# Optimization experiments

Measured on AMD Instinct MI355X. Metric: run time of the kernel, lower is better.

## Reference

```python
import jax, jax.numpy as jnp
import numpy as np

N = 50000          # nodes
E = 800000         # edges (before self-loops)
DIN = 1024         # input_dim_mel
HID = 128          # hidden_dim
HEADS = 2
NC = 4             # num_classes
NEG_SLOPE = 0.2    # PyG GATConv default


def setup_inputs() -> dict:
    key = jax.random.key(0)
    ks = jax.random.split(key, 12)
    s = 0.05
    return {
        "x": jax.random.normal(ks[0], (N, DIN), dtype=jnp.float32),
        "edge_index": jax.random.randint(ks[1], (2, E), 0, N, dtype=jnp.int64),
        # linear_pre (stored as [in, out])
        "W_pre": jax.random.normal(ks[2], (DIN, HID), dtype=jnp.float32) * s,
        "b_pre": jnp.zeros((HID,), dtype=jnp.float32),
        # gat1: GATConv(HID, HID, heads=2, concat=True)
        "W1": jax.random.normal(ks[3], (HID, HEADS * HID), dtype=jnp.float32) * s,
        "a_src1": jax.random.normal(ks[4], (HEADS, HID), dtype=jnp.float32) * s,
        "a_dst1": jax.random.normal(ks[5], (HEADS, HID), dtype=jnp.float32) * s,
        "b1": jnp.zeros((HEADS * HID,), dtype=jnp.float32),
        # gat2: GATConv(HID*HEADS, NC, heads=1, concat=True)
        "W2": jax.random.normal(ks[6], (HEADS * HID, NC), dtype=jnp.float32) * s,
        "a_src2": jax.random.normal(ks[7], (1, NC), dtype=jnp.float32) * s,
        "a_dst2": jax.random.normal(ks[8], (1, NC), dtype=jnp.float32) * s,
        "b2": jnp.zeros((NC,), dtype=jnp.float32),
    }


def _gat_conv(x, W, a_src, a_dst, bias, src, dst, heads, out_ch):
    """PyG GATConv (concat=True, self-loops already appended to src/dst)."""
    n = x.shape[0]
    h = (x @ W).reshape(n, heads, out_ch)            # [N,H,C]
    alpha_src = (h * a_src).sum(-1)                  # [N,H]
    alpha_dst = (h * a_dst).sum(-1)                  # [N,H]
    e = alpha_src[src] + alpha_dst[dst]              # [E,H] edge scores
    e = jax.nn.leaky_relu(e, NEG_SLOPE)
    # segment softmax over incoming edges of each dst node
    m = jax.ops.segment_max(e, dst, num_segments=n)  # [N,H]
    e = jnp.exp(e - m[dst])
    s = jax.ops.segment_sum(e, dst, num_segments=n)  # [N,H]
    alpha = e / (s[dst] + 1e-16)                     # [E,H]
    # gather src messages, weight by attention, scatter-add to dst
    out = jax.ops.segment_sum(h[src] * alpha[:, :, None], dst, num_segments=n)
    return out.reshape(n, heads * out_ch) + bias


def reference(x, edge_index, W_pre, b_pre, W1, a_src1, a_dst1, b1,
              W2, a_src2, a_dst2, b2):
    n = x.shape[0]
    # add self-loops (PyG GATConv default)
    loops = jnp.arange(n, dtype=edge_index.dtype)
    src = jnp.concatenate([edge_index[0], loops])
    dst = jnp.concatenate([edge_index[1], loops])

    h = jax.nn.relu(x @ W_pre + b_pre)                               # [N,HID]
    h = jax.nn.elu(_gat_conv(h, W1, a_src1, a_dst1, b1, src, dst, HEADS, HID))
    out = _gat_conv(h, W2, a_src2, a_dst2, b2, src, dst, 1, NC)      # [N,NC]
    return out
```

## Files before the change

kernel.cpp:

```cpp
#include <hip/hip_runtime.h>
#include <hip/hip_bf16.h>

#define NEG_SLOPE 0.2f

typedef _Float16 f16x8 __attribute__((ext_vector_type(8)));
typedef _Float16 f16x4 __attribute__((ext_vector_type(4)));
typedef float f32x4 __attribute__((ext_vector_type(4)));
typedef unsigned short ushort_t;

#define AS_GLOBAL(p) ((const __attribute__((address_space(1))) void*)(p))
#define AS_SHARED(p) ((__attribute__((address_space(3))) void*)(p))

__device__ inline f16x4 cvt4(float4 v) {
    f16x4 r;
    r[0] = (_Float16)v.x; r[1] = (_Float16)v.y;
    r[2] = (_Float16)v.z; r[3] = (_Float16)v.w;
    return r;
}

__global__ __launch_bounds__(256) void kl1(const int* __restrict__ edst, int E,
                                           int* __restrict__ counts,
                                           const float* __restrict__ Wpre,
                                           const float* __restrict__ W1,
                                           ushort_t* __restrict__ PreF,
                                           ushort_t* __restrict__ W1h, int HB) {
    int b = blockIdx.x, t = threadIdx.x;
    if (b < HB) {
        int i = b * 256 + t;
        if (i < E) atomicAdd(&counts[edst[i]], 1);
    } else {
        int i = (b - HB) * 256 + t;
        if (i < 1024 * 128) {
            int k = i >> 7, n = i & 127;
            int d = ((k >> 3) * 128 + n) * 8 + (k & 7);
            PreF[d] = __builtin_bit_cast(ushort_t, (_Float16)Wpre[i]);
        } else if (i < 1024 * 128 + 128 * 256) {
            int j2 = i - 1024 * 128;
            int k = j2 >> 8, n = j2 & 255;
            int d = ((k >> 3) * 256 + n) * 8 + (k & 7);
            W1h[d] = __builtin_bit_cast(ushort_t, (_Float16)W1[j2]);
        }
    }
}

__global__ __launch_bounds__(256) void kl2(const float* __restrict__ A,
                                           const ushort_t* __restrict__ Bf,
                                           const float* __restrict__ bias,
                                           ushort_t* __restrict__ C, int M,
                                           const int* __restrict__ counts,
                                           int* __restrict__ row_ptr,
                                           int* __restrict__ cursor) {
    __shared__ __align__(16) ushort_t Bs[8192];
    __shared__ __align__(16) ushort_t As[2048];
    __shared__ int wsum2[4];
    int t = threadIdx.x;

    if (blockIdx.x == 0) {
        int CH = (M + 255) >> 8;
        int lo = t * CH, hi = min(lo + CH, M);
        int s = 0;
        for (int i = lo; i < hi; ++i) s += counts[i] + 1;
        int lane = t & 63, wid = t >> 6;
        int x = s;
        #pragma unroll
        for (int off = 1; off < 64; off <<= 1) {
            int y = __shfl_up(x, off, 64);
            if (lane >= off) x += y;
        }
        if (lane == 63) wsum2[wid] = x;
        __syncthreads();
        int wof = 0;
        #pragma unroll
        for (int w = 0; w < 3; ++w) if (wid > w) wof += wsum2[w];
        int run = wof + x - s;
        for (int i = lo; i < hi; ++i) {
            row_ptr[i] = run;
            cursor[i] = run;
            run += counts[i] + 1;
        }
        if (lo < M && hi == M) row_ptr[M] = run;
        return;
    }

    int wid = t >> 6, lane = t & 63, q = lane >> 4, l15 = lane & 15;
    int wr = wid & 1, wc = wid >> 1;
    int m0 = (blockIdx.x - 1) * 32;

    int ar = t >> 3, ac = t & 7;
    int srow = m0 + ar;
    if (srow >= M) srow = M - 1;
    const float* sA = A + (size_t)srow * 1024;
    int sw = ar & 7;
    int wadr0 = ar * 64 + (((ac >> 1)) ^ sw) * 8 + (ac & 1) * 4;
    int wadr1 = ar * 64 + ((4 + (ac >> 1)) ^ sw) * 8 + (ac & 1) * 4;

    float4 av[2][2];
    av[0][0] = *(const float4*)(sA + ac * 4);
    av[0][1] = *(const float4*)(sA + 32 + ac * 4);

    f32x4 acc[4];
    #pragma unroll
    for (int c = 0; c < 4; ++c) acc[c] = (f32x4){0.f, 0.f, 0.f, 0.f};

    int arow_rd = (wr * 16 + l15) * 64;
    int asw = l15 & 7;

    #pragma unroll 2
    for (int kt = 0; kt < 16; ++kt) {
        int cur = kt & 1, nxt = cur ^ 1;
        __syncthreads();
        {
            const ushort_t* sF = Bf + kt * 8192;
            #pragma unroll
            for (int i = 0; i < 4; ++i) {
                int ge = (i * 256 + t) * 8;
                int le = (i * 256 + (t & 0xC0)) * 8;
                __builtin_amdgcn_global_load_lds(AS_GLOBAL(sF + ge), AS_SHARED(Bs + le), 16, 0, 0);
            }
        }
        if (kt < 15) {
            const float* a2 = sA + (kt + 1) * 64;
            av[nxt][0] = *(const float4*)(a2 + ac * 4);
            av[nxt][1] = *(const float4*)(a2 + 32 + ac * 4);
        }
        *(f16x4*)(As + wadr0) = cvt4(av[cur][0]);
        *(f16x4*)(As + wadr1) = cvt4(av[cur][1]);
        __syncthreads();
        #pragma unroll
        for (int ks = 0; ks < 2; ++ks) {
            int kc = ks * 4 + q;
            f16x8 af = *(const f16x8*)(As + arow_rd + ((kc ^ asw) * 8));
            #pragma unroll
            for (int c = 0; c < 4; ++c) {
                f16x8 b = *(const f16x8*)(Bs + (kc * 128 + wc * 64 + c * 16 + l15) * 8);
                acc[c] = __builtin_amdgcn_mfma_f32_16x16x32_f16(af, b, acc[c], 0, 0, 0);
            }
        }
    }
    #pragma unroll
    for (int c = 0; c < 4; ++c) {
        int n = wc * 64 + c * 16 + l15;
        float bv = bias[n];
        #pragma unroll
        for (int r = 0; r < 4; ++r) {
            int mm = m0 + wr * 16 + q * 4 + r;
            if (mm < M)
                C[(size_t)mm * 128 + n] =
                    __builtin_bit_cast(ushort_t, (_Float16)fmaxf(acc[c][r] + bv, 0.f));
        }
    }
}

__global__ __launch_bounds__(256) void kl3(const int* __restrict__ esrc,
                                           const int* __restrict__ edst, int E, int n,
                                           int* __restrict__ cursor,
                                           int* __restrict__ edge_src, int FB,
                                           const ushort_t* __restrict__ Ah,
                                           const ushort_t* __restrict__ W1h,
                                           const float* __restrict__ a_src,
                                           const float* __restrict__ a_dst,
                                           ushort_t* __restrict__ C,
                                           float* __restrict__ as1,
                                           float* __restrict__ ad1, int M) {
    __shared__ __align__(16) ushort_t Bs[16384];
    int t = threadIdx.x;
    int b = blockIdx.x;
    if (b < FB) {
        int i = b * 256 + t;
        if (i < E) {
            int p = atomicAdd(&cursor[edst[i]], 1);
            edge_src[p] = esrc[i];
        } else if (i < E + n) {
            int v = i - E;
            int p = atomicAdd(&cursor[v], 1);
            edge_src[p] = v;
        }
        return;
    }
    int u = b - FB;
    int g = u & 1;
    int mblk = u >> 1;
    int wid = t >> 6, lane = t & 63;
    int q = lane >> 4, l15 = lane & 15;
    int m0 = mblk * 64 + wid * 16;
    int m = m0 + l15;
    const ushort_t* arow = Ah + (size_t)(m < M ? m : 0) * 128;

    {
        #pragma unroll
        for (int i = 0; i < 8; ++i) {
            int j = i * 4 + wid;
            int kc = j >> 1, hk = j & 1;
            int ge = ((kc * 256) + g * 128 + hk * 64 + lane) * 8;
            int le = j * 512;
            __builtin_amdgcn_global_load_lds(AS_GLOBAL(W1h + ge), AS_SHARED(Bs + le), 16, 0, 0);
        }
    }
    f16x8 af[4];
    #pragma unroll
    for (int ks = 0; ks < 4; ++ks)
        af[ks] = *(const f16x8*)(arow + ks * 32 + q * 8);
    __syncthreads();

    f32x4 acc[8];
    #pragma unroll
    for (int c = 0; c < 8; ++c) acc[c] = (f32x4){0.f, 0.f, 0.f, 0.f};

    #pragma unroll
    for (int ks = 0; ks < 4; ++ks) {
        int kc = ks * 4 + q;
        #pragma unroll
        for (int c = 0; c < 8; ++c) {
            f16x8 bfr = *(const f16x8*)(Bs + (kc * 128 + c * 16 + l15) * 8);
            acc[c] = __builtin_amdgcn_mfma_f32_16x16x32_f16(af[ks], bfr, acc[c], 0, 0, 0);
        }
    }
    #pragma unroll
    for (int c = 0; c < 8; ++c) {
        int nn = g * 128 + c * 16 + l15;
        #pragma unroll
        for (int r = 0; r < 4; ++r) {
            int mm = m0 + q * 4 + r;
            if (mm < M)
                C[(size_t)mm * 256 + nn] = __builtin_bit_cast(ushort_t, (_Float16)acc[c][r]);
        }
    }
    float asv[4] = {0.f, 0.f, 0.f, 0.f};
    float adv[4] = {0.f, 0.f, 0.f, 0.f};
    #pragma unroll
    for (int c = 0; c < 8; ++c) {
        float sa = a_src[g * 128 + c * 16 + l15];
        float da = a_dst[g * 128 + c * 16 + l15];
        #pragma unroll
        for (int r = 0; r < 4; ++r) {
            asv[r] += acc[c][r] * sa;
            adv[r] += acc[c][r] * da;
        }
    }
    #pragma unroll
    for (int off = 1; off <= 8; off <<= 1) {
        #pragma unroll
        for (int r = 0; r < 4; ++r) {
            asv[r] += __shfl_xor(asv[r], off, 64);
            adv[r] += __shfl_xor(adv[r], off, 64);
        }
    }
    if (l15 == 0) {
        #pragma unroll
        for (int r = 0; r < 4; ++r) {
            int node = m0 + q * 4 + r;
            if (node < M) {
                as1[node * 2 + g] = asv[r];
                ad1[node * 2 + g] = adv[r];
            }
        }
    }
}

__global__ __launch_bounds__(256) void kagg1(const ushort_t* __restrict__ h1h,
                                             const float* __restrict__ as1,
                                             const float* __restrict__ ad1,
                                             const float* __restrict__ b1,
                                             const float* __restrict__ W2,
                                             const float* __restrict__ a_src2,
                                             const float* __restrict__ a_dst2,
                                             const int* __restrict__ row_ptr,
                                             const int* __restrict__ edge_src,
                                             float* __restrict__ h2,
                                             float* __restrict__ as2,
                                             float* __restrict__ ad2, int n) {
    int wid = threadIdx.x >> 6, lane = threadIdx.x & 63;
    int node = blockIdx.x * 4 + wid;
    if (node >= n) return;
    int beg = row_ptr[node], end = row_ptr[node + 1];
    int h = lane >> 5;
    float adv0 = ad1[node * 2];
    float adv1 = ad1[node * 2 + 1];
    float acc0 = 0.f, acc1 = 0.f, acc2 = 0.f, acc3 = 0.f, ssum = 0.f;
    for (int base = beg; base < end; base += 32) {
        int cnt = min(32, end - base);
        float wv_mine = 0.f;
        int s_mine = 0;
        {
            int i = lane >> 1, hh = lane & 1;
            if (i < cnt) {
                s_mine = edge_src[base + i];
                float e = as1[s_mine * 2 + hh] + (hh ? adv1 : adv0);
                e = (e > 0.f) ? e : NEG_SLOPE * e;
                wv_mine = __expf(e);
            }
        }
        #pragma unroll 4
        for (int i2 = 0; i2 < cnt; ++i2) {
            int s = __shfl(s_mine, i2 * 2, 64);
            float wv = __shfl(wv_mine, i2 * 2 + h, 64);
            uint2 p = *(const uint2*)(h1h + (size_t)s * 256 + lane * 4);
            acc0 += wv * (float)__builtin_bit_cast(_Float16, (ushort_t)(p.x & 0xffffu));
            acc1 += wv * (float)__builtin_bit_cast(_Float16, (ushort_t)(p.x >> 16));
            acc2 += wv * (float)__builtin_bit_cast(_Float16, (ushort_t)(p.y & 0xffffu));
            acc3 += wv * (float)__builtin_bit_cast(_Float16, (ushort_t)(p.y >> 16));
            ssum += wv;
        }
    }
    float inv = 1.f / (ssum + 1e-16f);
    float o0 = acc0 * inv + b1[lane * 4 + 0];
    float o1 = acc1 * inv + b1[lane * 4 + 1];
    float o2 = acc2 * inv + b1[lane * 4 + 2];
    float o3 = acc3 * inv + b1[lane * 4 + 3];
    o0 = (o0 > 0.f) ? o0 : (__expf(o0) - 1.f);
    o1 = (o1 > 0.f) ? o1 : (__expf(o1) - 1.f);
    o2 = (o2 > 0.f) ? o2 : (__expf(o2) - 1.f);
    o3 = (o3 > 0.f) ? o3 : (__expf(o3) - 1.f);
    float4 w0 = *(const float4*)(W2 + (lane * 4 + 0) * 4);
    float4 w1 = *(const float4*)(W2 + (lane * 4 + 1) * 4);
    float4 w2 = *(const float4*)(W2 + (lane * 4 + 2) * 4);
    float4 w3 = *(const float4*)(W2 + (lane * 4 + 3) * 4);
    float p0 = o0 * w0.x + o1 * w1.x + o2 * w2.x + o3 * w3.x;
    float p1 = o0 * w0.y + o1 * w1.y + o2 * w2.y + o3 * w3.y;
    float p2 = o0 * w0.z + o1 * w1.z + o2 * w2.z + o3 * w3.z;
    float p3 = o0 * w0.w + o1 * w1.w + o2 * w2.w + o3 * w3.w;
    #pragma unroll
    for (int off = 1; off < 64; off <<= 1) {
        p0 += __shfl_xor(p0, off, 64);
        p1 += __shfl_xor(p1, off, 64);
        p2 += __shfl_xor(p2, off, 64);
        p3 += __shfl_xor(p3, off, 64);
    }
    if (lane == 0) {
        h2[node * 4 + 0] = p0;
        h2[node * 4 + 1] = p1;
        h2[node * 4 + 2] = p2;
        h2[node * 4 + 3] = p3;
        as2[node] = p0 * a_src2[0] + p1 * a_src2[1] + p2 * a_src2[2] + p3 * a_src2[3];
        ad2[node] = p0 * a_dst2[0] + p1 * a_dst2[1] + p2 * a_dst2[2] + p3 * a_dst2[3];
    }
}

__global__ __launch_bounds__(256) void kagg2(const float* __restrict__ h2,
                                             const float* __restrict__ as2,
                                             const float* __restrict__ ad2,
                                             const float* __restrict__ b2,
                                             const int* __restrict__ row_ptr,
                                             const int* __restrict__ edge_src,
                                             float* __restrict__ out, int n) {
    int wid = threadIdx.x >> 6, lane = threadIdx.x & 63;
    int node = blockIdx.x * 4 + wid;
    if (node >= n) return;
    int beg = row_ptr[node], end = row_ptr[node + 1];
    int j = lane & 3, ig = lane >> 2;
    float adv = ad2[node];
    float acc = 0.f, ssum = 0.f;
    for (int p = beg + ig; p < end; p += 16) {
        int s = edge_src[p];
        float e = as2[s] + adv;
        e = (e > 0.f) ? e : NEG_SLOPE * e;
        float wv = __expf(e);
        acc += wv * h2[s * 4 + j];
        ssum += wv;
    }
    #pragma unroll
    for (int off = 32; off >= 4; off >>= 1) {
        acc += __shfl_down(acc, off);
        ssum += __shfl_down(ssum, off);
    }
    if (lane < 4) out[node * 4 + j] = acc / (ssum + 1e-16f) + b2[j];
}

extern "C" void kernel_launch(void* const* d_in, const int* in_sizes, int n_in,
                              void* d_out, int out_size, void* d_ws, size_t ws_size,
                              hipStream_t stream) {
    const float* x      = (const float*)d_in[0];
    const int*   ei     = (const int*)d_in[1];
    const float* W_pre  = (const float*)d_in[2];
    const float* b_pre  = (const float*)d_in[3];
    const float* W1     = (const float*)d_in[4];
    const float* a_src1 = (const float*)d_in[5];
    const float* a_dst1 = (const float*)d_in[6];
    const float* b1     = (const float*)d_in[7];
    const float* W2     = (const float*)d_in[8];
    const float* a_src2 = (const float*)d_in[9];
    const float* a_dst2 = (const float*)d_in[10];
    const float* b2     = (const float*)d_in[11];
    float* out = (float*)d_out;

    const int DIN = 1024;
    const int E = in_sizes[1] / 2;
    const int N = in_sizes[0] / DIN;

    const int* esrc = ei;
    const int* edst = ei + E;

    char* ws = (char*)d_ws;
    size_t off = 0;
    ushort_t* h1h = (ushort_t*)(ws + off); off += (size_t)N * 256 * 2;
    ushort_t* h0h = (ushort_t*)(ws + off); off += (size_t)N * 128 * 2;
    float* as1 = (float*)(ws + off);  off += (size_t)N * 2 * 4;
    float* ad1 = (float*)(ws + off);  off += (size_t)N * 2 * 4;
    float* h2  = (float*)(ws + off);  off += (size_t)N * 4 * 4;
    float* as2 = (float*)(ws + off);  off += (size_t)N * 4;
    float* ad2 = (float*)(ws + off);  off += (size_t)N * 4;
    int* row_ptr = (int*)(ws + off);  off += ((size_t)N + 16) * 4;
    int* cursor  = (int*)(ws + off);  off += (size_t)N * 4;
    int* counts  = (int*)(ws + off);  off += (size_t)N * 4;
    int* edge_src = (int*)(ws + off); off += (size_t)(E + N) * 4;
    ushort_t* PreF = (ushort_t*)(ws + off); off += 1024 * 128 * 2;
    ushort_t* W1h  = (ushort_t*)(ws + off); off += 128 * 256 * 2;

    hipMemsetAsync(counts, 0, (size_t)N * 4, stream);

    int HB = (E + 255) / 256;
    kl1<<<HB + 640, 256, 0, stream>>>(edst, E, counts, W_pre, W1, PreF, W1h, HB);

    int Mb32 = (N + 31) / 32;
    kl2<<<1 + Mb32, 256, 0, stream>>>(x, PreF, b_pre, h0h, N, counts, row_ptr, cursor);

    int FB = (E + N + 255) / 256;
    int Mb = (N + 63) / 64;
    kl3<<<FB + 2 * Mb, 256, 0, stream>>>(esrc, edst, E, N, cursor, edge_src, FB,
                                         h0h, W1h, a_src1, a_dst1, h1h, as1, ad1, N);

    kagg1<<<(N + 3) / 4, 256, 0, stream>>>(h1h, as1, ad1, b1, W2, a_src2, a_dst2,
                                           row_ptr, edge_src, h2, as2, ad2, N);
    kagg2<<<(N + 3) / 4, 256, 0, stream>>>(h2, as2, ad2, b2, row_ptr, edge_src, out, N);
}
```

Measured before the change: 609.6 us.

## Parallelize CSR prefix scan, pre-place self-loops, batch gathers in aggregation

Replaces the single-block serial prefix scan that was folded into the GEMM launch with a two-kernel multi-block scan. The second kernel also writes each node's self-loop into the first slot of its row, so the edge-fill no longer needs atomics for self-loops. The layer-1 aggregation loop now issues 8 neighbor gathers before doing the arithmetic, to raise memory-level parallelism. The cost is two extra kernel launches, and the scan no longer overlaps with the GEMM blocks.

```diff
diff --git a/kernel.cpp b/kernel.cpp
--- a/kernel.cpp
+++ b/kernel.cpp
@@ -43,48 +43,76 @@
     }
 }
 
-__global__ __launch_bounds__(256) void kl2(const float* __restrict__ A,
-                                           const ushort_t* __restrict__ Bf,
-                                           const float* __restrict__ bias,
-                                           ushort_t* __restrict__ C, int M,
-                                           const int* __restrict__ counts,
-                                           int* __restrict__ row_ptr,
-                                           int* __restrict__ cursor) {
+__global__ __launch_bounds__(1024) void kscan_part(const int* __restrict__ counts,
+                                                   int* __restrict__ row_ptr,
+                                                   int* __restrict__ bsum, int n) {
+    __shared__ int wsum[16];
+    int t = threadIdx.x, lane = t & 63, wid = t >> 6;
+    int i = blockIdx.x * 1024 + t;
+    int v = (i < n) ? (counts[i] + 1) : 0;
+    int x = v;
+    #pragma unroll
+    for (int off = 1; off < 64; off <<= 1) {
+        int y = __shfl_up(x, off, 64);
+        if (lane >= off) x += y;
+    }
+    if (lane == 63) wsum[wid] = x;
+    __syncthreads();
+    if (wid == 0) {
+        int ws = (lane < 16) ? wsum[lane] : 0;
+        #pragma unroll
+        for (int off = 1; off < 16; off <<= 1) {
+            int y = __shfl_up(ws, off, 64);
+            if (lane >= off) ws += y;
+        }
+        if (lane < 16) wsum[lane] = ws;
+    }
+    __syncthreads();
+    int wave_excl = (wid == 0) ? 0 : wsum[wid - 1];
+    if (i < n) row_ptr[i] = wave_excl + (x - v);
+    if (t == 0) bsum[blockIdx.x] = wsum[15];
+}
+
+__global__ __launch_bounds__(256) void kscan_add(int* __restrict__ row_ptr,
+                                                 const int* __restrict__ bsum,
+                                                 int* __restrict__ cursor,
+                                                 int* __restrict__ edge_src,
+                                                 int n, int G) {
+    __shared__ int s_off;
+    int t = threadIdx.x;
+    int chunk = blockIdx.x >> 2;
+    if (t < 64) {
+        int v = (t < G && t < chunk) ? bsum[t] : 0;
+        #pragma unroll
+        for (int off = 32; off >= 1; off >>= 1) v += __shfl_down(v, off, 64);
+        if (t == 0) s_off = v;
+    }
+    __syncthreads();
+    int i = blockIdx.x * 256 + t;
+    if (i < n) {
+        int r = row_ptr[i] + s_off;
+        row_ptr[i] = r;
+        cursor[i] = r + 1;
+        edge_src[r] = i;
+    }
+    if (blockIdx.x == 0 && t < 64) {
+        int v = (t < G) ? bsum[t] : 0;
+        #pragma unroll
+        for (int off = 32; off >= 1; off >>= 1) v += __shfl_down(v, off, 64);
+        if (t == 0) row_ptr[n] = v;
+    }
+}
+
+__global__ __launch_bounds__(256) void kgemm_mfma1(const float* __restrict__ A,
+                                                   const ushort_t* __restrict__ Bf,
+                                                   const float* __restrict__ bias,
+                                                   ushort_t* __restrict__ C, int M) {
     __shared__ __align__(16) ushort_t Bs[8192];
     __shared__ __align__(16) ushort_t As[2048];
-    __shared__ int wsum2[4];
     int t = threadIdx.x;
-
-    if (blockIdx.x == 0) {
-        int CH = (M + 255) >> 8;
-        int lo = t * CH, hi = min(lo + CH, M);
-        int s = 0;
-        for (int i = lo; i < hi; ++i) s += counts[i] + 1;
-        int lane = t & 63, wid = t >> 6;
-        int x = s;
-        #pragma unroll
-        for (int off = 1; off < 64; off <<= 1) {
-            int y = __shfl_up(x, off, 64);
-            if (lane >= off) x += y;
-        }
-        if (lane == 63) wsum2[wid] = x;
-        __syncthreads();
-        int wof = 0;
-        #pragma unroll
-        for (int w = 0; w < 3; ++w) if (wid > w) wof += wsum2[w];
-        int run = wof + x - s;
-        for (int i = lo; i < hi; ++i) {
-            row_ptr[i] = run;
-            cursor[i] = run;
-            run += counts[i] + 1;
-        }
-        if (lo < M && hi == M) row_ptr[M] = run;
-        return;
-    }
-
     int wid = t >> 6, lane = t & 63, q = lane >> 4, l15 = lane & 15;
     int wr = wid & 1, wc = wid >> 1;
-    int m0 = (blockIdx.x - 1) * 32;
+    int m0 = blockIdx.x * 32;
 
     int ar = t >> 3, ac = t & 7;
     int srow = m0 + ar;
@@ -152,7 +180,7 @@
 }
 
 __global__ __launch_bounds__(256) void kl3(const int* __restrict__ esrc,
-                                           const int* __restrict__ edst, int E, int n,
+                                           const int* __restrict__ edst, int E,
                                            int* __restrict__ cursor,
                                            int* __restrict__ edge_src, int FB,
                                            const ushort_t* __restrict__ Ah,
@@ -170,10 +198,6 @@
         if (i < E) {
             int p = atomicAdd(&cursor[edst[i]], 1);
             edge_src[p] = esrc[i];
-        } else if (i < E + n) {
-            int v = i - E;
-            int p = atomicAdd(&cursor[v], 1);
-            edge_src[p] = v;
         }
         return;
     }
@@ -290,16 +314,28 @@
                 wv_mine = __expf(e);
             }
         }
-        #pragma unroll 4
-        for (int i2 = 0; i2 < cnt; ++i2) {
-            int s = __shfl(s_mine, i2 * 2, 64);
-            float wv = __shfl(wv_mine, i2 * 2 + h, 64);
-            uint2 p = *(const uint2*)(h1h + (size_t)s * 256 + lane * 4);
-            acc0 += wv * (float)__builtin_bit_cast(_Float16, (ushort_t)(p.x & 0xffffu));
-            acc1 += wv * (float)__builtin_bit_cast(_Float16, (ushort_t)(p.x >> 16));
-            acc2 += wv * (float)__builtin_bit_cast(_Float16, (ushort_t)(p.y & 0xffffu));
-            acc3 += wv * (float)__builtin_bit_cast(_Float16, (ushort_t)(p.y >> 16));
-            ssum += wv;
+        for (int i0 = 0; i0 < cnt; i0 += 8) {
+            uint2 pv[8];
+            float wv8[8];
+            #pragma unroll
+            for (int j = 0; j < 8; ++j) {
+                int idx = i0 + j;
+                int sr = __shfl(s_mine, idx * 2, 64);
+                float wr = __shfl(wv_mine, idx * 2 + h, 64);
+                int ok = idx < cnt;
+                int s = ok ? sr : 0;
+                wv8[j] = ok ? wr : 0.f;
+                pv[j] = *(const uint2*)(h1h + (size_t)s * 256 + lane * 4);
+            }
+            #pragma unroll
+            for (int j = 0; j < 8; ++j) {
+                float wv = wv8[j];
+                acc0 += wv * (float)__builtin_bit_cast(_Float16, (ushort_t)(pv[j].x & 0xffffu));
+                acc1 += wv * (float)__builtin_bit_cast(_Float16, (ushort_t)(pv[j].x >> 16));
+                acc2 += wv * (float)__builtin_bit_cast(_Float16, (ushort_t)(pv[j].y & 0xffffu));
+                acc3 += wv * (float)__builtin_bit_cast(_Float16, (ushort_t)(pv[j].y >> 16));
+                ssum += wv;
+            }
         }
     }
     float inv = 1.f / (ssum + 1e-16f);
@@ -402,21 +438,27 @@
     int* row_ptr = (int*)(ws + off);  off += ((size_t)N + 16) * 4;
     int* cursor  = (int*)(ws + off);  off += (size_t)N * 4;
     int* counts  = (int*)(ws + off);  off += (size_t)N * 4;
+    int* bsum    = (int*)(ws + off);  off += 64 * 4;
     int* edge_src = (int*)(ws + off); off += (size_t)(E + N) * 4;
     ushort_t* PreF = (ushort_t*)(ws + off); off += 1024 * 128 * 2;
     ushort_t* W1h  = (ushort_t*)(ws + off); off += 128 * 256 * 2;
 
+    int G = (N + 1023) / 1024;
+
     hipMemsetAsync(counts, 0, (size_t)N * 4, stream);
 
     int HB = (E + 255) / 256;
     kl1<<<HB + 640, 256, 0, stream>>>(edst, E, counts, W_pre, W1, PreF, W1h, HB);
 
+    kscan_part<<<G, 1024, 0, stream>>>(counts, row_ptr, bsum, N);
+    kscan_add<<<(N + 255) / 256, 256, 0, stream>>>(row_ptr, bsum, cursor, edge_src, N, G);
+
     int Mb32 = (N + 31) / 32;
-    kl2<<<1 + Mb32, 256, 0, stream>>>(x, PreF, b_pre, h0h, N, counts, row_ptr, cursor);
-
-    int FB = (E + N + 255) / 256;
+    kgemm_mfma1<<<Mb32, 256, 0, stream>>>(x, PreF, b_pre, h0h, N);
+
+    int FB = (E + 255) / 256;
     int Mb = (N + 63) / 64;
-    kl3<<<FB + 2 * Mb, 256, 0, stream>>>(esrc, edst, E, N, cursor, edge_src, FB,
+    kl3<<<FB + 2 * Mb, 256, 0, stream>>>(esrc, edst, E, cursor, edge_src, FB,
                                          h0h, W1h, a_src1, a_dst1, h1h, as1, ad1, N);
 
     kagg1<<<(N + 3) / 4, 256, 0, stream>>>(h1h, as1, ad1, b1, W2, a_src2, a_dst2,
```

Result: faster. 507.2 us (-16.8%).
